# Kernel optimization log

Measured on AMD Instinct MI355X. Metric: run time of the kernel, lower is better.

Reference implementation:

```python
import jax, jax.numpy as jnp
import numpy as np

HEADS = 8
CHANNELS = 256
RR = 1
DH = CHANNELS // RR                 # per-head channels
ATT = HEADS * DH                    # 2048
# exact scale from the torch module
SCALE = (1.0 / np.sqrt(CHANNELS // RR)) / np.sqrt(2.0 / (CHANNELS + 3 * ATT)) * np.sqrt(2.0 / (CHANNELS + ATT))


def setup_inputs() -> dict:
    key = jax.random.key(0)
    k1, k2, k3, k4, k5 = jax.random.split(key, 5)
    x = jax.random.normal(k1, (8, CHANNELS, 32, 32), dtype=jnp.float32)
    # 1x1 conv weights stored as [out_ch, in_ch]
    w_in = jax.random.normal(k2, (3 * ATT, CHANNELS), dtype=jnp.float32) * (1.0 / np.sqrt(CHANNELS))
    b_in = jax.random.normal(k3, (3 * ATT,), dtype=jnp.float32) * 0.02
    w_out = jax.random.normal(k4, (CHANNELS, ATT), dtype=jnp.float32) * (1.0 / np.sqrt(ATT))
    b_out = jax.random.normal(k5, (CHANNELS,), dtype=jnp.float32) * 0.02
    return {"x": x, "w_in": w_in, "b_in": b_in, "w_out": w_out, "b_out": b_out}


def reference(x, w_in, b_in, w_out, b_out):
    n, c, h, w = x.shape
    L = h * w
    xf = x.reshape(n, c, L)
    # 1x1 conv in = channel-mixing matmul, then fixed scale
    scaled = (jnp.einsum('ncl,oc->nol', xf, w_in) + b_in[:, None]) * jnp.float32(SCALE)
    s = scaled.reshape(n, HEADS, 3 * DH, L)
    q, k, v = s[:, :, :DH], s[:, :, DH:2 * DH], s[:, :, 2 * DH:]   # each (n, H, DH, L)
    att = jnp.einsum('nhdl,nhdm->nhlm', q, k)                       # (n, H, L, L)
    # softmax over the FLATTENED L*L axis (global per head), as in the torch code
    att = jax.nn.softmax(att.reshape(n, HEADS, L * L), axis=2).reshape(n, HEADS, L, L)
    out = jnp.einsum('nhdl,nhlm->nhdm', v, att)                     # (n, H, DH, L)
    out = out.reshape(n, ATT, L)
    out = jnp.einsum('nal,ca->ncl', out, w_out) + b_out[:, None]
    return out.reshape(n, c, h, w)
```

## Files before the change

kernel.cpp:

```cpp
#include <hip/hip_runtime.h>
#include <hip/hip_bf16.h>


typedef __bf16 bf16x8 __attribute__((ext_vector_type(8)));
typedef __bf16 bf16x4 __attribute__((ext_vector_type(4)));
typedef float f32x4 __attribute__((ext_vector_type(4)));
typedef float f32x16 __attribute__((ext_vector_type(16)));
typedef __hip_bfloat16 bf16;

__device__ __forceinline__ void async_copy16(const void* g, void* s) {
    __builtin_amdgcn_global_load_lds(
        (const __attribute__((address_space(1))) unsigned int*)g,
        (__attribute__((address_space(3))) unsigned int*)s, 16, 0, 0);
}

__device__ __forceinline__ bf16x8 scale8(bf16x8 v, float s) {
    bf16x8 r;
#pragma unroll
    for (int e = 0; e < 8; ++e) r[e] = (__bf16)((float)v[e] * s);
    return r;
}

__global__ __launch_bounds__(256)
void proj_qkv(const bf16* __restrict__ Axw, const bf16* __restrict__ Wsw,
              const float* __restrict__ bias, float scale,
              bf16* __restrict__ outQ, bf16* __restrict__ outK, bf16* __restrict__ outV)
{
    __shared__ __align__(16) bf16 smem[16384];

    const int tid  = threadIdx.x;
    const int wave = tid >> 6, lane = tid & 63;
    const int l31  = lane & 31, hw = lane >> 5;

    const int b  = blockIdx.x;
    const int n  = b & 7;
    const int s  = b >> 3;
    const int ht = s / 48;
    const int r_ = s % 48;
    const int part = r_ % 6;
    const int lt   = r_ / 6;
    const int nh = n * 8 + ht;
    const int o0 = ht * 768 + part * 128;
    const int d0 = (part & 1) * 128;

    const int wl = wave & 1, wo = wave >> 1;

    const bf16* Ap0 = Axw + ((long)(n * 32 + lt * 4 + wl * 2) * 16) * 512 + lane * 8;
    const bf16* Ap1 = Ap0 + 16 * 512;
    const bf16* Bp0 = Wsw + ((long)(ht * 24 + part * 4 + wo * 2) * 16) * 512 + lane * 8;
    const bf16* Bp1 = Bp0 + 16 * 512;

    bf16x8 Af[3][2], Bf[3][2];
#pragma unroll
    for (int p = 0; p < 3; ++p) {
        Af[p][0] = *(const bf16x8*)(Ap0 + p * 512);
        Af[p][1] = *(const bf16x8*)(Ap1 + p * 512);
        Bf[p][0] = *(const bf16x8*)(Bp0 + p * 512);
        Bf[p][1] = *(const bf16x8*)(Bp1 + p * 512);
    }

    f32x16 acc[2][2] = {};
#pragma unroll
    for (int k = 0; k < 16; ++k) {
        const int st = k % 3;
#pragma unroll
        for (int i = 0; i < 2; ++i)
#pragma unroll
            for (int j = 0; j < 2; ++j)
                acc[i][j] = __builtin_amdgcn_mfma_f32_32x32x16_bf16(
                    Af[st][i], Bf[st][j], acc[i][j], 0, 0, 0);
        if (k + 3 < 16) {
            Af[st][0] = *(const bf16x8*)(Ap0 + (k + 3) * 512);
            Af[st][1] = *(const bf16x8*)(Ap1 + (k + 3) * 512);
            Bf[st][0] = *(const bf16x8*)(Bp0 + (k + 3) * 512);
            Bf[st][1] = *(const bf16x8*)(Bp1 + (k + 3) * 512);
        }
    }

    float bv[2];
#pragma unroll
    for (int j = 0; j < 2; ++j) bv[j] = bias[o0 + wo * 64 + j * 32 + l31];

    if (part < 4) {
#pragma unroll
        for (int i = 0; i < 2; ++i)
#pragma unroll
            for (int j = 0; j < 2; ++j)
#pragma unroll
                for (int r = 0; r < 16; ++r) {
                    const int row = wl * 64 + i * 32 + (r & 3) + 8 * (r >> 2) + 4 * hw;
                    const int col = wo * 64 + j * 32 + l31;
                    const float v = (acc[i][j][r] + bv[j]) * scale;
                    const int c32 = col >> 3;
                    const int slot = (c32 & 8) | ((c32 & 7) ^ (row & 7));
                    smem[row * 128 + slot * 8 + (col & 7)] = __float2bfloat16(v);
                }
        __syncthreads();
        bf16* dst = (part < 2) ? outQ : outK;
#pragma unroll
        for (int k = 0; k < 8; ++k) {
            const int flat = k * 256 + tid;
            const int seg  = flat >> 6, ln = flat & 63;
            const int lb   = seg >> 3, wloc = seg & 7;
            const int row  = lb * 32 + (ln & 31);
            const int c32  = wloc * 2 + (ln >> 5);
            const int slot = (c32 & 8) | ((c32 & 7) ^ (row & 7));
            const f32x4 val = *(const f32x4*)(smem + row * 128 + slot * 8);
            const long addr = ((long)(nh * 32 + lt * 4 + lb) * 16 + (d0 >> 4) + wloc) * 512 + ln * 8;
            *(f32x4*)(dst + addr) = val;
        }
    } else {
#pragma unroll
        for (int i = 0; i < 2; ++i)
#pragma unroll
            for (int j = 0; j < 2; ++j)
#pragma unroll
                for (int r = 0; r < 16; ++r) {
                    const int row = wl * 64 + i * 32 + (r & 3) + 8 * (r >> 2) + 4 * hw;
                    const int col = wo * 64 + j * 32 + l31;
                    const float v = (acc[i][j][r] + bv[j]) * scale;
                    const int rc = row >> 3;
                    const int slotT = (rc & 8) | ((rc & 7) ^ (col & 7));
                    smem[col * 128 + slotT * 8 + (row & 7)] = __float2bfloat16(v);
                }
        __syncthreads();
#pragma unroll
        for (int k = 0; k < 8; ++k) {
            const int flat = k * 256 + tid;
            const int seg  = flat >> 6, ln = flat & 63;
            const int kwl  = seg >> 2, g2l = seg & 3;
            const int dl   = g2l * 32 + (ln & 31);
            const int lc   = kwl * 2 + (ln >> 5);
            const int slotT = (lc & 8) | ((lc & 7) ^ (dl & 7));
            const f32x4 val = *(const f32x4*)(smem + dl * 128 + slotT * 8);
            const long addr = ((long)(nh * 64 + lt * 8 + kwl) * 8 + (d0 >> 5) + g2l) * 512 + ln * 8;
            *(f32x4*)(outV + addr) = val;
        }
    }
}

__global__ __launch_bounds__(256)
void gemm_nt(const bf16* __restrict__ A, const bf16* __restrict__ B, void* __restrict__ Cvoid,
             int M, int N, int K, int lda, int ldb, int ldc,
             long asn, long ash, long bsn, long bsh, long csn, long csh,
             int H, int mode, const float* __restrict__ bias, const float* __restrict__ Zp,
             float scale)
{
    __shared__ __align__(16) bf16 smem[17408];
    bf16* Alds = smem;
    bf16* Blds = smem + 8192;

    const int tid  = threadIdx.x;
    const int wave = tid >> 6;
    const int lane = tid & 63;
    const int z  = blockIdx.z;
    const int zn = z / H, zh = z % H;

    const bf16* Ab = A + zn * asn + zh * ash;
    const bf16* Bb = B + zn * bsn + zh * bsh;

    const long tM = (long)blockIdx.y * 128;
    const long tN = (long)blockIdx.x * 128;

    const int wr   = (wave >> 1) * 64;
    const int wc   = (wave & 1) * 64;
    const int l15  = lane & 15;
    const int quad = lane >> 4;

    f32x4 acc[4][4] = {};

    const int kiters = K >> 6;
    const bool regB = (mode == 4);

#pragma unroll
    for (int i = 0; i < 4; ++i) {
        const int flat = i * 256 + tid;
        const int row  = flat >> 3;
        const int kcs  = (flat & 7) ^ (row & 7);
        async_copy16(Ab + (tM + row) * (long)lda + kcs * 8,
                     (char*)Alds + (long)(i * 256 + wave * 64) * 16);
        if (!regB) {
            async_copy16(Bb + (tN + row) * (long)ldb + kcs * 8,
                         (char*)Blds + (long)(i * 256 + wave * 64) * 16);
        }
    }
    if (regB) {
        const float zi0 = 1.0f / Zp[zn * 8 + zh * 4];
#pragma unroll
        for (int i = 0; i < 4; ++i) {
            const int flat = i * 256 + tid;
            const int row  = flat >> 3;
            const int kcs  = (flat & 7) ^ (row & 7);
            bf16x8 bv = *(const bf16x8*)(Bb + (tN + row) * (long)ldb + kcs * 8);
            *(bf16x8*)((char*)Blds + (long)flat * 16) = scale8(bv, zi0);
        }
    }

    bf16x8 pfA[4], pfB[4];
    for (int kt = 0; kt < kiters; ++kt) {
        __syncthreads();
        const bool has_next = (kt + 1 < kiters);
        float zin = 1.0f;
        if (has_next) {
            const long kof = (long)(kt + 1) * 64;
            if (regB) zin = 1.0f / Zp[zn * 8 + zh * 4 + ((kt + 1) >> 2)];
#pragma unroll
            for (int i = 0; i < 4; ++i) {
                const int flat = i * 256 + tid;
                const int row  = flat >> 3;
                const int kcs  = (flat & 7) ^ (row & 7);
                pfA[i] = *(const bf16x8*)(Ab + (tM + row) * (long)lda + kof + kcs * 8);
                pfB[i] = *(const bf16x8*)(Bb + (tN + row) * (long)ldb + kof + kcs * 8);
            }
        }
#pragma unroll
        for (int kk = 0; kk < 2; ++kk) {
            bf16x8 af[4], bfv[4];
#pragma unroll
            for (int i = 0; i < 4; ++i) {
                const int r = wr + i * 16 + l15;
                af[i] = *(const bf16x8*)(Alds + r * 64 + ((kk * 4 + quad) ^ (r & 7)) * 8);
            }
#pragma unroll
            for (int j = 0; j < 4; ++j) {
                const int r = wc + j * 16 + l15;
                bfv[j] = *(const bf16x8*)(Blds + r * 64 + ((kk * 4 + quad) ^ (r & 7)) * 8);
            }
#pragma unroll
            for (int i = 0; i < 4; ++i)
#pragma unroll
                for (int j = 0; j < 4; ++j)
                    acc[i][j] = __builtin_amdgcn_mfma_f32_16x16x32_bf16(af[i], bfv[j], acc[i][j], 0, 0, 0);
        }
        if (has_next) {
            __builtin_amdgcn_sched_barrier(0);
            __builtin_amdgcn_s_barrier();
            __builtin_amdgcn_sched_barrier(0);
#pragma unroll
            for (int i = 0; i < 4; ++i) {
                const int flat = i * 256 + tid;
                *(bf16x8*)((char*)Alds + (long)flat * 16) = pfA[i];
                *(bf16x8*)((char*)Blds + (long)flat * 16) = regB ? scale8(pfB[i], zin) : pfB[i];
            }
        }
    }

    float* C = (float*)Cvoid + zn * csn + zh * csh;
#pragma unroll
    for (int i = 0; i < 4; ++i)
#pragma unroll
        for (int j = 0; j < 4; ++j)
#pragma unroll
            for (int r = 0; r < 4; ++r) {
                const long row = tM + wr + i * 16 + quad * 4 + r;
                const long col = tN + wc + j * 16 + l15;
                if (mode == 4) {
                    const float v = acc[i][j][r] + (zh == 0 ? bias[row] : 0.0f);
                    atomicAdd(&C[row * (long)ldc + col], v);
                } else {
                    C[row * (long)ldc + col] = acc[i][j][r] + bias[row];
                }
            }
}

__global__ __launch_bounds__(256, 2)
void attn_fused(const bf16* __restrict__ Qsw, const bf16* __restrict__ Ksw,
                const bf16* __restrict__ Vsw, bf16* __restrict__ out_tt,
                float* __restrict__ Z)
{
    __shared__ __align__(16) bf16 smem[16904];
    bf16* Ps  = smem;
    float* Zs = (float*)(smem + 16896);

    const int tid  = threadIdx.x;
    const int wave = tid >> 6, lane = tid & 63;
    const int l31  = lane & 31, hw = lane >> 5;

    const int b   = blockIdx.x;
    const int xcd = b & 7, s = b >> 3;
    const int nh  = xcd * 8 + (s >> 4);
    const int mt  = s & 15;
    const int n   = nh >> 3, h = nh & 7;
    const long m0 = (long)mt * 64;

    const int wl = wave & 1, wm = wave >> 1;

    bf16x8 Kf[16];
    {
        const bf16* kb = Ksw + ((long)(nh * 32 + mt * 2 + wm) * 16) * 512 + lane * 8;
#pragma unroll
        for (int w = 0; w < 16; ++w)
            Kf[w] = *(const bf16x8*)(kb + w * 512);
    }
    bf16x8 Qc[16];
    {
        const bf16* qb = Qsw + ((long)(nh * 32 + wl) * 16) * 512 + lane * 8;
#pragma unroll
        for (int w = 0; w < 16; ++w)
            Qc[w] = *(const bf16x8*)(qb + w * 512);
    }

    f32x16 accO[2][2] = {};
    float zsum = 0.0f;

    for (int lt = 0; lt < 16; ++lt) {
        bf16x8 vf[4][2];
#pragma unroll
        for (int kw = 0; kw < 4; ++kw)
#pragma unroll
            for (int dt = 0; dt < 2; ++dt)
                vf[kw][dt] = *(const bf16x8*)(
                    Vsw + ((long)(nh * 64 + lt * 4 + kw) * 8 + wave * 2 + dt) * 512 + lane * 8);

        f32x16 a0 = {}, a1 = {};
#pragma unroll
        for (int w = 0; w < 16; w += 2) {
            a0 = __builtin_amdgcn_mfma_f32_32x32x16_bf16(Qc[w], Kf[w], a0, 0, 0, 0);
            a1 = __builtin_amdgcn_mfma_f32_32x32x16_bf16(Qc[w + 1], Kf[w + 1], a1, 0, 0, 0);
        }

        bf16* Pb = Ps + (lt & 1) * 6144;
#pragma unroll
        for (int g = 0; g < 4; ++g) {
            bf16x4 pk;
#pragma unroll
            for (int e = 0; e < 4; ++e) {
                const float v = __expf(a0[g * 4 + e] + a1[g * 4 + e]);
                zsum += v;
                pk[e] = (__bf16)v;
            }
            const int l  = wl * 32 + 4 * hw + 8 * g;
            const int kw = l >> 4, off = l & 15;
            *(bf16x4*)(Pb + kw * 1536 + (wm * 32 + l31) * 24 + off) = pk;
        }

        __syncthreads();

        if (lt < 15) {
            const bf16* qn = Qsw + ((long)(nh * 32 + (lt + 1) * 2 + wl) * 16) * 512 + lane * 8;
#pragma unroll
            for (int w = 0; w < 16; ++w)
                Qc[w] = *(const bf16x8*)(qn + w * 512);
        }

#pragma unroll
        for (int kw = 0; kw < 4; ++kw) {
            bf16x8 pf[2];
#pragma unroll
            for (int mh = 0; mh < 2; ++mh)
                pf[mh] = *(const bf16x8*)(Pb + kw * 1536 + (mh * 32 + l31) * 24 + hw * 8);
#pragma unroll
            for (int mh = 0; mh < 2; ++mh)
#pragma unroll
                for (int dt = 0; dt < 2; ++dt)
                    accO[mh][dt] = __builtin_amdgcn_mfma_f32_32x32x16_bf16(
                        pf[mh], vf[kw][dt], accO[mh][dt], 0, 0, 0);
        }
    }

    __syncthreads();

#pragma unroll
    for (int o = 32; o > 0; o >>= 1) zsum += __shfl_down(zsum, o);
    if (lane == 0) Zs[wave] = zsum;

    bf16* Cs = smem;
#pragma unroll
    for (int mh = 0; mh < 2; ++mh)
#pragma unroll
        for (int dt = 0; dt < 2; ++dt)
#pragma unroll
            for (int r = 0; r < 16; ++r) {
                const int m = mh * 32 + (r & 3) + 8 * (r >> 2) + 4 * hw;
                const int d = wave * 64 + dt * 32 + l31;
                Cs[m * 264 + d] = __float2bfloat16(accO[mh][dt][r]);
            }
    __syncthreads();
    if (tid == 0) atomicAdd(Z + nh, (Zs[0] + Zs[1]) + (Zs[2] + Zs[3]));

    bf16* Ob = out_tt + (long)n * 2097152 + m0 * 2048 + h * 256;
#pragma unroll
    for (int k = 0; k < 8; ++k) {
        const int flat = k * 256 + tid;
        const int row  = flat >> 5;
        const int c    = flat & 31;
        const f32x4 val = *(const f32x4*)((const char*)Cs + row * 528 + c * 16);
        *(f32x4*)((char*)(Ob + (long)row * 2048) + c * 16) = val;
    }
}

__global__ void prep_convert(const float* __restrict__ w_in, const float* __restrict__ w_out,
                             bf16* __restrict__ Wsw, bf16* __restrict__ w_out_b,
                             float* __restrict__ Z, float* __restrict__ out)
{
    const long gid = (long)blockIdx.x * 256 + threadIdx.x;
    if (blockIdx.x == 0 && threadIdx.x < 64) Z[threadIdx.x] = 0.0f;
    const f32x4 z4 = {0.0f, 0.0f, 0.0f, 0.0f};
    if (gid < 524288) ((f32x4*)out)[gid] = z4;
    const long n1 = 6144L * 256;
    const long n2 = 256L * 2048;
    const long stride = (long)gridDim.x * 256;
    for (long i = gid; i < n1; i += stride) {
        const int o = (int)(i >> 8), c = (int)(i & 255);
        const long addr = ((long)((o >> 5) * 16 + (c >> 4))) * 512
                        + ((o & 31) + 32 * ((c >> 3) & 1)) * 8 + (c & 7);
        Wsw[addr] = __float2bfloat16(w_in[i]);
    }
    for (long i = gid; i < n2; i += stride) w_out_b[i] = __float2bfloat16(w_out[i]);
}

__global__ void prep_xt(const float* __restrict__ x, bf16* __restrict__ Axw)
{
    __shared__ float tile[64][65];
    const int b = blockIdx.x;
    const int n = blockIdx.y;
    const int ct = b & 3, lt = b >> 2;
    const int t = threadIdx.x;
    const float* xp = x + (long)n * 256 * 1024;
#pragma unroll
    for (int i = 0; i < 16; ++i) {
        const int flat = i * 256 + t;
        const int cl = flat >> 6, ll = flat & 63;
        tile[cl][ll] = xp[(long)(ct * 64 + cl) * 1024 + lt * 64 + ll];
    }
    __syncthreads();
#pragma unroll
    for (int i = 0; i < 16; ++i) {
        const int flat = i * 256 + t;
        const int lr = flat >> 6, cr = flat & 63;
        const int l = lt * 64 + lr, c = ct * 64 + cr;
        const long addr = ((long)((n * 32 + (l >> 5)) * 16 + (c >> 4))) * 512
                        + ((l & 31) + 32 * ((c >> 3) & 1)) * 8 + (c & 7);
        Axw[addr] = __float2bfloat16(tile[cr][lr]);
    }
}

extern "C" void kernel_launch(void* const* d_in, const int* in_sizes, int n_in,
                              void* d_out, int out_size, void* d_ws, size_t ws_size,
                              hipStream_t stream)
{
    const float* x     = (const float*)d_in[0];
    const float* w_in  = (const float*)d_in[1];
    const float* b_in  = (const float*)d_in[2];
    const float* w_out = (const float*)d_in[3];
    const float* b_out = (const float*)d_in[4];
    float* out = (float*)d_out;

    const float SCALE = 0.10416666666666667f;

    char* p = (char*)d_ws;
    bf16* Qsw     = (bf16*)p;  p += 33554432;
    bf16* Ksw     = (bf16*)p;  p += 33554432;
    bf16* Vsw     = (bf16*)p;  p += 33554432;
    bf16* out_tt  = (bf16*)p;  p += 33554432;
    bf16* Axw     = (bf16*)p;  p += 4194304;
    bf16* Wsw     = (bf16*)p;  p += 3145728;
    bf16* w_out_b = (bf16*)p;  p += 1048576;
    float* Z      = (float*)p; p += 256;

    prep_convert<<<2048, 256, 0, stream>>>(w_in, w_out, Wsw, w_out_b, Z, out);
    prep_xt<<<dim3(64, 8), 256, 0, stream>>>(x, Axw);

    proj_qkv<<<3072, 256, 0, stream>>>(Axw, Wsw, b_in, SCALE, Qsw, Ksw, Vsw);

    attn_fused<<<1024, 256, 0, stream>>>(Qsw, Ksw, Vsw, out_tt, Z);

    gemm_nt<<<dim3(8, 2, 16), 256, 0, stream>>>(
        w_out_b, out_tt, out,
        256, 1024, 1024, 2048, 2048, 1024,
        0, 1024, 1024L * 2048, 1024, 256L * 1024, 0,
        2, 4, b_out, Z, 1.0f);
}
```

Baseline: 239.6 us.

## Software-pipeline attention loop: overlap QK^T of next tile with PV of previous

Restructures the attention main loop into a prologue/steady-state/epilogue pipeline. Each iteration computes the QK^T scores for tile lt and consumes the P tile from lt-1 (double-buffered in LDS), so only one barrier is needed per iteration. The exp/store runs after the MFMAs, and V loads are issued a step ahead. MFMA sections are wrapped in s_setprio to favour matrix issue. Keeping an extra f32x16 score set and V fragments live raises register pressure.

```diff
diff --git a/kernel.cpp b/kernel.cpp
--- a/kernel.cpp
+++ b/kernel.cpp
@@ -299,27 +299,33 @@
         for (int w = 0; w < 16; ++w)
             Qc[w] = *(const bf16x8*)(qb + w * 512);
     }
+    bf16x8 vf[4][2];
+#pragma unroll
+    for (int kw = 0; kw < 4; ++kw)
+#pragma unroll
+        for (int dt = 0; dt < 2; ++dt)
+            vf[kw][dt] = *(const bf16x8*)(
+                Vsw + ((long)(nh * 64 + kw) * 8 + wave * 2 + dt) * 512 + lane * 8);
 
     f32x16 accO[2][2] = {};
     float zsum = 0.0f;
 
-    for (int lt = 0; lt < 16; ++lt) {
-        bf16x8 vf[4][2];
-#pragma unroll
-        for (int kw = 0; kw < 4; ++kw)
-#pragma unroll
-            for (int dt = 0; dt < 2; ++dt)
-                vf[kw][dt] = *(const bf16x8*)(
-                    Vsw + ((long)(nh * 64 + lt * 4 + kw) * 8 + wave * 2 + dt) * 512 + lane * 8);
-
+    {
         f32x16 a0 = {}, a1 = {};
+        __builtin_amdgcn_s_setprio(1);
 #pragma unroll
         for (int w = 0; w < 16; w += 2) {
             a0 = __builtin_amdgcn_mfma_f32_32x32x16_bf16(Qc[w], Kf[w], a0, 0, 0, 0);
             a1 = __builtin_amdgcn_mfma_f32_32x32x16_bf16(Qc[w + 1], Kf[w + 1], a1, 0, 0, 0);
         }
-
-        bf16* Pb = Ps + (lt & 1) * 6144;
+        __builtin_amdgcn_s_setprio(0);
+        {
+            const bf16* qn = Qsw + ((long)(nh * 32 + 2 + wl) * 16) * 512 + lane * 8;
+#pragma unroll
+            for (int w = 0; w < 16; ++w)
+                Qc[w] = *(const bf16x8*)(qn + w * 512);
+        }
+        bf16* Pb = Ps;
 #pragma unroll
         for (int g = 0; g < 4; ++g) {
             bf16x4 pk;
@@ -333,22 +339,32 @@
             const int kw = l >> 4, off = l & 15;
             *(bf16x4*)(Pb + kw * 1536 + (wm * 32 + l31) * 24 + off) = pk;
         }
-
         __syncthreads();
-
+    }
+
+    for (int lt = 1; lt < 16; ++lt) {
+        const bf16* Pp = Ps + ((lt - 1) & 1) * 6144;
+        bf16* Pb = Ps + (lt & 1) * 6144;
+
+        f32x16 a0 = {}, a1 = {};
+        __builtin_amdgcn_s_setprio(1);
+#pragma unroll
+        for (int w = 0; w < 16; w += 2) {
+            a0 = __builtin_amdgcn_mfma_f32_32x32x16_bf16(Qc[w], Kf[w], a0, 0, 0, 0);
+            a1 = __builtin_amdgcn_mfma_f32_32x32x16_bf16(Qc[w + 1], Kf[w + 1], a1, 0, 0, 0);
+        }
         if (lt < 15) {
             const bf16* qn = Qsw + ((long)(nh * 32 + (lt + 1) * 2 + wl) * 16) * 512 + lane * 8;
 #pragma unroll
             for (int w = 0; w < 16; ++w)
                 Qc[w] = *(const bf16x8*)(qn + w * 512);
         }
-
 #pragma unroll
         for (int kw = 0; kw < 4; ++kw) {
             bf16x8 pf[2];
 #pragma unroll
             for (int mh = 0; mh < 2; ++mh)
-                pf[mh] = *(const bf16x8*)(Pb + kw * 1536 + (mh * 32 + l31) * 24 + hw * 8);
+                pf[mh] = *(const bf16x8*)(Pp + kw * 1536 + (mh * 32 + l31) * 24 + hw * 8);
 #pragma unroll
             for (int mh = 0; mh < 2; ++mh)
 #pragma unroll
@@ -356,6 +372,49 @@
                     accO[mh][dt] = __builtin_amdgcn_mfma_f32_32x32x16_bf16(
                         pf[mh], vf[kw][dt], accO[mh][dt], 0, 0, 0);
         }
+        __builtin_amdgcn_s_setprio(0);
+
+#pragma unroll
+        for (int kw = 0; kw < 4; ++kw)
+#pragma unroll
+            for (int dt = 0; dt < 2; ++dt)
+                vf[kw][dt] = *(const bf16x8*)(
+                    Vsw + ((long)(nh * 64 + lt * 4 + kw) * 8 + wave * 2 + dt) * 512 + lane * 8);
+
+#pragma unroll
+        for (int g = 0; g < 4; ++g) {
+            bf16x4 pk;
+#pragma unroll
+            for (int e = 0; e < 4; ++e) {
+                const float v = __expf(a0[g * 4 + e] + a1[g * 4 + e]);
+                zsum += v;
+                pk[e] = (__bf16)v;
+            }
+            const int l  = wl * 32 + 4 * hw + 8 * g;
+            const int kw = l >> 4, off = l & 15;
+            *(bf16x4*)(Pb + kw * 1536 + (wm * 32 + l31) * 24 + off) = pk;
+        }
+
+        __syncthreads();
+    }
+
+    {
+        const bf16* Pp = Ps + 6144;
+        __builtin_amdgcn_s_setprio(1);
+#pragma unroll
+        for (int kw = 0; kw < 4; ++kw) {
+            bf16x8 pf[2];
+#pragma unroll
+            for (int mh = 0; mh < 2; ++mh)
+                pf[mh] = *(const bf16x8*)(Pp + kw * 1536 + (mh * 32 + l31) * 24 + hw * 8);
+#pragma unroll
+            for (int mh = 0; mh < 2; ++mh)
+#pragma unroll
+                for (int dt = 0; dt < 2; ++dt)
+                    accO[mh][dt] = __builtin_amdgcn_mfma_f32_32x32x16_bf16(
+                        pf[mh], vf[kw][dt], accO[mh][dt], 0, 0, 0);
+        }
+        __builtin_amdgcn_s_setprio(0);
     }
 
     __syncthreads();
```

New measurement: 262.1 us. 9.4% more time.
